# Kernel tuning notes

Hardware: AMD Instinct MI355X
Metric: run time of the kernel (lower is better)

The kernel has to match this reference:

```python
import jax, jax.numpy as jnp
import numpy as np

N = 6144      # nodes
NFEAT = 512
NHID = 256
NHEADS = 4
DHEAD = NHID // NHEADS  # 64
NEMBED = 128
NEG_INF = -9e15
LRELU_ALPHA = 0.2


def setup_inputs() -> dict:
    key = jax.random.key(0)
    k = jax.random.split(key, 8)
    x = jax.random.normal(k[0], (N, NFEAT), dtype=jnp.float32)
    adj = (jax.random.uniform(k[1], (N, N)) < 0.01).astype(jnp.int32)
    # per-head GAT params, packed over heads
    W = jax.random.normal(k[2], (NHEADS, NFEAT, DHEAD), dtype=jnp.float32) * 0.05
    a_src = jax.random.normal(k[3], (NHEADS, DHEAD), dtype=jnp.float32) * 0.05
    a_dst = jax.random.normal(k[4], (NHEADS, DHEAD), dtype=jnp.float32) * 0.05
    # output linear (init.normal_ std=0.05 per reset_parameters)
    lin_w = jax.random.normal(k[5], (NEMBED, NHID), dtype=jnp.float32) * 0.05
    lin_b = jnp.zeros((NEMBED,), dtype=jnp.float32)
    return {"x": x, "adj": adj, "W": W, "a_src": a_src, "a_dst": a_dst,
            "lin_w": lin_w, "lin_b": lin_b}


def _gat_forward(x, adj, W, a_src, a_dst, lin_w, lin_b):
    # Wh: [H, N, D]
    Wh = jnp.einsum('nf,hfd->hnd', x, W)
    # attention logits e_ij = leakyrelu(a_src.Wh_i + a_dst.Wh_j): [H, N, N]
    s = jnp.einsum('hnd,hd->hn', Wh, a_src)   # source term per node
    t = jnp.einsum('hnd,hd->hn', Wh, a_dst)   # target term per node
    e = s[:, :, None] + t[:, None, :]
    e = jax.nn.leaky_relu(e, negative_slope=LRELU_ALPHA)
    # mask by adjacency, softmax over neighbors
    e = jnp.where(adj[None, :, :] > 0, e, NEG_INF)
    attn = jax.nn.softmax(e, axis=-1)
    # aggregate and per-head ELU (concat=True GAT layer)
    h = jnp.einsum('hnm,hmd->hnd', attn, Wh)
    h = jax.nn.elu(h)
    # concat heads -> [N, NHID]
    h = jnp.transpose(h, (1, 0, 2)).reshape(N, NHID)
    # dropout is identity in eval mode; linear + ELU
    out = jax.nn.elu(h @ lin_w.T + lin_b)
    return out


def reference(x, adj, W, a_src, a_dst, lin_w, lin_b):
    return _gat_forward(x, adj, W, a_src, a_dst, lin_w, lin_b)
```

## Files before the change

kernel.cpp:

```cpp
#include <hip/hip_runtime.h>
#include <hip/hip_bf16.h>
#include <math.h>

#define N_NODES 6144
#define NFEAT 512
#define NHID 256
#define NHEADS 4
#define DHEAD 64
#define NEMBED 128
#define LRELU_ALPHA 0.2f
#define MAXC 256
#define ASTRIDE 20

__global__ __launch_bounds__(256) void gemm_scan(const float* __restrict__ x,
                                                 const float* __restrict__ W,
                                                 const float* __restrict__ a_src,
                                                 const float* __restrict__ a_dst,
                                                 const int* __restrict__ adj,
                                                 float* __restrict__ Wh,
                                                 float* __restrict__ s_arr,
                                                 float* __restrict__ t_arr,
                                                 int* __restrict__ cnt_g,
                                                 unsigned short* __restrict__ nbr_g) {
    __shared__ float As[64][ASTRIDE];
    __shared__ float Bs[16][64];
    const int tid = threadIdx.x;

    if (blockIdx.y < NHEADS) {
        const int tx = tid & 15;
        const int ty = tid >> 4;
        const int row0 = blockIdx.x * 64;
        const int h = blockIdx.y;
        const float* Bp = W + (size_t)h * NFEAT * DHEAD;

        float acc[4][4] = {};

        for (int k0 = 0; k0 < NFEAT; k0 += 16) {
            {
                const int r = tid >> 2, kq = tid & 3;
                const float4 v = *(const float4*)(x + (size_t)(row0 + r) * NFEAT + k0 + kq * 4);
                *(float4*)&As[r][kq * 4] = v;
            }
            {
                const int kk = tid >> 4, cq = tid & 15;
                const float4 v = *(const float4*)(Bp + (size_t)(k0 + kk) * DHEAD + cq * 4);
                *(float4*)&Bs[kk][cq * 4] = v;
            }
            __syncthreads();
#pragma unroll
            for (int kk = 0; kk < 16; kk++) {
                float a[4], b[4];
#pragma unroll
                for (int i = 0; i < 4; i++) a[i] = As[ty * 4 + i][kk];
#pragma unroll
                for (int j = 0; j < 4; j++) b[j] = Bs[kk][tx * 4 + j];
#pragma unroll
                for (int i = 0; i < 4; i++)
#pragma unroll
                    for (int j = 0; j < 4; j++) acc[i][j] += a[i] * b[j];
            }
            __syncthreads();
        }
#pragma unroll
        for (int i = 0; i < 4; i++) {
            const int row = row0 + ty * 4 + i;
            float4 v = make_float4(acc[i][0], acc[i][1], acc[i][2], acc[i][3]);
            *(float4*)(Wh + ((size_t)h * N_NODES + row) * DHEAD + tx * 4) = v;
        }
        float a4s[4], a4d[4];
#pragma unroll
        for (int j = 0; j < 4; j++) {
            a4s[j] = a_src[h * DHEAD + tx * 4 + j];
            a4d[j] = a_dst[h * DHEAD + tx * 4 + j];
        }
#pragma unroll
        for (int i = 0; i < 4; i++) {
            float ps = acc[i][0] * a4s[0] + acc[i][1] * a4s[1] +
                       acc[i][2] * a4s[2] + acc[i][3] * a4s[3];
            float pt = acc[i][0] * a4d[0] + acc[i][1] * a4d[1] +
                       acc[i][2] * a4d[2] + acc[i][3] * a4d[3];
#pragma unroll
            for (int off = 1; off < 16; off <<= 1) {
                ps += __shfl_xor(ps, off);
                pt += __shfl_xor(pt, off);
            }
            if (tx == 0) {
                const int row = row0 + ty * 4 + i;
                s_arr[h * N_NODES + row] = ps;
                t_arr[h * N_NODES + row] = pt;
            }
        }
    } else {
        const int r = (blockIdx.y - NHEADS) * gridDim.x + blockIdx.x;
        const int* arow = adj + (size_t)r * N_NODES;
        unsigned short* nrow = nbr_g + (size_t)r * MAXC;
        int* cp = cnt_g + r;

        int4 v[6];
#pragma unroll
        for (int it = 0; it < 6; ++it)
            v[it] = *(const int4*)(arow + it * 1024 + tid * 4);

#pragma unroll
        for (int it = 0; it < 6; ++it) {
            const int j0 = it * 1024 + tid * 4;
            const int n = (v[it].x != 0) + (v[it].y != 0) + (v[it].z != 0) + (v[it].w != 0);
            if (n) {
                int base = atomicAdd(cp, n);
                if (v[it].x) { if (base < MAXC) nrow[base] = (unsigned short)j0; ++base; }
                if (v[it].y) { if (base < MAXC) nrow[base] = (unsigned short)(j0 + 1); ++base; }
                if (v[it].z) { if (base < MAXC) nrow[base] = (unsigned short)(j0 + 2); ++base; }
                if (v[it].w) { if (base < MAXC) nrow[base] = (unsigned short)(j0 + 3); }
            }
        }
    }
}

__global__ __launch_bounds__(256) void attn_agg(const int* __restrict__ adj,
                                                const float* __restrict__ Wh,
                                                const float* __restrict__ s_arr,
                                                const float* __restrict__ t_arr,
                                                const int* __restrict__ cnt_g,
                                                const unsigned short* __restrict__ nbr_g,
                                                float* __restrict__ hcat) {
    __shared__ unsigned short nbr[MAXC];
    __shared__ float p_s[NHEADS][MAXC];
    const int i = blockIdx.x;
    const int tid = threadIdx.x;
    const int h = tid >> 6;
    const int lane = tid & 63;
    const int c = cnt_g[i];
    const float* whp = Wh + (size_t)h * N_NODES * DHEAD;

    float acc, l;
    if (c > 0 && c <= MAXC) {
        for (int k = tid; k < c; k += 256) nbr[k] = nbr_g[(size_t)i * MAXC + k];
        __syncthreads();

        const float s_h = s_arr[h * N_NODES + i];
        const float* tp = t_arr + (size_t)h * N_NODES;
        float m = -INFINITY;
        for (int k = lane; k < c; k += 64) {
            float e = s_h + tp[nbr[k]];
            e = e >= 0.0f ? e : LRELU_ALPHA * e;
            p_s[h][k] = e;
            m = fmaxf(m, e);
        }
#pragma unroll
        for (int off = 32; off > 0; off >>= 1) m = fmaxf(m, __shfl_xor(m, off));
        float ls = 0.0f;
        for (int k = lane; k < c; k += 64) {
            const float p = __expf(p_s[h][k] - m);
            p_s[h][k] = p;
            ls += p;
        }
#pragma unroll
        for (int off = 32; off > 0; off >>= 1) ls += __shfl_xor(ls, off);
        l = ls;

        float a0 = 0.f, a1 = 0.f, a2 = 0.f, a3 = 0.f;
        float a4 = 0.f, a5 = 0.f, a6 = 0.f, a7 = 0.f;
        int k = 0;
        for (; k + 8 <= c; k += 8) {
            const int j0 = nbr[k],     j1 = nbr[k + 1], j2 = nbr[k + 2], j3 = nbr[k + 3];
            const int j4 = nbr[k + 4], j5 = nbr[k + 5], j6 = nbr[k + 6], j7 = nbr[k + 7];
            const float p0 = p_s[h][k],     p1 = p_s[h][k + 1];
            const float p2 = p_s[h][k + 2], p3 = p_s[h][k + 3];
            const float p4 = p_s[h][k + 4], p5 = p_s[h][k + 5];
            const float p6 = p_s[h][k + 6], p7 = p_s[h][k + 7];
            a0 += p0 * whp[(size_t)j0 * DHEAD + lane];
            a1 += p1 * whp[(size_t)j1 * DHEAD + lane];
            a2 += p2 * whp[(size_t)j2 * DHEAD + lane];
            a3 += p3 * whp[(size_t)j3 * DHEAD + lane];
            a4 += p4 * whp[(size_t)j4 * DHEAD + lane];
            a5 += p5 * whp[(size_t)j5 * DHEAD + lane];
            a6 += p6 * whp[(size_t)j6 * DHEAD + lane];
            a7 += p7 * whp[(size_t)j7 * DHEAD + lane];
        }
        for (; k < c; k++) a0 += p_s[h][k] * whp[(size_t)nbr[k] * DHEAD + lane];
        acc = ((a0 + a1) + (a2 + a3)) + ((a4 + a5) + (a6 + a7));
    } else if (c == 0) {
        acc = 0.0f;
        for (int j = 0; j < N_NODES; j++) acc += whp[(size_t)j * DHEAD + lane];
        l = (float)N_NODES;
    } else {
        const int* arow = adj + (size_t)i * N_NODES;
        const float s_h = s_arr[h * N_NODES + i];
        const float* tp = t_arr + (size_t)h * N_NODES;
        float m = -INFINITY, ll = 0.0f;
        acc = 0.0f;
        for (int j = 0; j < N_NODES; j++) {
            if (arow[j]) {
                float e = s_h + tp[j];
                e = e >= 0.0f ? e : LRELU_ALPHA * e;
                const float m_new = fmaxf(m, e);
                const float scale = __expf(m - m_new);
                const float p = __expf(e - m_new);
                ll = ll * scale + p;
                acc = acc * scale + p * whp[(size_t)j * DHEAD + lane];
                m = m_new;
            }
        }
        l = ll;
    }
    float hv = acc / l;
    hv = hv > 0.0f ? hv : expm1f(hv);
    hcat[(size_t)i * NHID + h * DHEAD + lane] = hv;
}

__global__ __launch_bounds__(256) void out_gemm(const float* __restrict__ hcat,
                                                const float* __restrict__ lin_w,
                                                const float* __restrict__ lin_b,
                                                float* __restrict__ out) {
    __shared__ float As[64][ASTRIDE * 4];
    __shared__ float Bs[16][64];
    const int tid = threadIdx.x;
    const int tx = tid & 15;
    const int ty = tid >> 4;
    const int row0 = blockIdx.x * 64;
    const int c0 = blockIdx.y * 64;

    float acc[4][4] = {};

    for (int k0 = 0; k0 < NHID; k0 += 16) {
        {
            const int r = tid >> 2, kq = tid & 3;
            const float4 v = *(const float4*)(hcat + (size_t)(row0 + r) * NHID + k0 + kq * 4);
            *(float4*)&As[r][kq * 4] = v;
        }
        {
            const int cc = tid & 63, kq = tid >> 6;
            const float4 v = *(const float4*)(lin_w + (size_t)(c0 + cc) * NHID + k0 + kq * 4);
            Bs[kq * 4 + 0][cc] = v.x;
            Bs[kq * 4 + 1][cc] = v.y;
            Bs[kq * 4 + 2][cc] = v.z;
            Bs[kq * 4 + 3][cc] = v.w;
        }
        __syncthreads();
#pragma unroll
        for (int kk = 0; kk < 16; kk++) {
            float a[4], b[4];
#pragma unroll
            for (int i = 0; i < 4; i++) a[i] = As[ty * 4 + i][kk];
#pragma unroll
            for (int j = 0; j < 4; j++) b[j] = Bs[kk][tx * 4 + j];
#pragma unroll
            for (int i = 0; i < 4; i++)
#pragma unroll
                for (int j = 0; j < 4; j++) acc[i][j] += a[i] * b[j];
        }
        __syncthreads();
    }
#pragma unroll
    for (int i = 0; i < 4; i++) {
        const int row = row0 + ty * 4 + i;
        float v[4];
#pragma unroll
        for (int j = 0; j < 4; j++) {
            const int col = c0 + tx * 4 + j;
            float val = acc[i][j] + lin_b[col];
            v[j] = val > 0.0f ? val : expm1f(val);
        }
        *(float4*)(out + (size_t)row * NEMBED + c0 + tx * 4) =
            make_float4(v[0], v[1], v[2], v[3]);
    }
}

extern "C" void kernel_launch(void* const* d_in, const int* in_sizes, int n_in,
                              void* d_out, int out_size, void* d_ws, size_t ws_size,
                              hipStream_t stream) {
    const float* x     = (const float*)d_in[0];
    const int*   adj   = (const int*)d_in[1];
    const float* W     = (const float*)d_in[2];
    const float* a_src = (const float*)d_in[3];
    const float* a_dst = (const float*)d_in[4];
    const float* lin_w = (const float*)d_in[5];
    const float* lin_b = (const float*)d_in[6];
    float* out = (float*)d_out;

    float* Wh   = (float*)d_ws;
    float* s    = Wh + (size_t)NHEADS * N_NODES * DHEAD;
    float* t    = s + (size_t)NHEADS * N_NODES;
    float* hcat = t + (size_t)NHEADS * N_NODES;
    int* cnt_g  = (int*)(hcat + (size_t)N_NODES * NHID);
    unsigned short* nbr_g = (unsigned short*)(cnt_g + N_NODES);

    hipMemsetAsync(cnt_g, 0, N_NODES * sizeof(int), stream);
    gemm_scan<<<dim3(96, NHEADS + 64), 256, 0, stream>>>(
        x, W, a_src, a_dst, adj, Wh, s, t, cnt_g, nbr_g);
    attn_agg<<<N_NODES, 256, 0, stream>>>(adj, Wh, s, t, cnt_g, nbr_g, hcat);
    out_gemm<<<dim3(N_NODES / 64, NEMBED / 64), 256, 0, stream>>>(hcat, lin_w, lin_b, out);
}
```

Measured before the change: 287.5 us.

## Transpose GEMM A tile for vector LDS reads and batch adjacency scan rows

The x tile is stored transposed in shared memory so each thread reads four A values with a single float4 LDS load instead of four scalar loads. The grid is flattened to 1D with the 384 GEMM blocks first. Each scan block now processes three adjacency rows and prefetches the next row's int4 data while compacting the current row, cutting scan blocks from 6144 to 2048. This aims to lower LDS instruction count in the GEMM and hide global-load latency in the memory-bound adjacency scan. The cost is more registers per scan thread and bank conflicts on the scalar transposed stores.

```diff
diff --git a/kernel.cpp b/kernel.cpp
--- a/kernel.cpp
+++ b/kernel.cpp
@@ -11,6 +11,9 @@
 #define LRELU_ALPHA 0.2f
 #define MAXC 256
 #define ASTRIDE 20
+#define GEMM_BLOCKS 384
+#define SCAN_BLOCKS 2048
+#define ROWS_PER_SCAN 3
 
 __global__ __launch_bounds__(256) void gemm_scan(const float* __restrict__ x,
                                                  const float* __restrict__ W,
@@ -22,15 +25,16 @@
                                                  float* __restrict__ t_arr,
                                                  int* __restrict__ cnt_g,
                                                  unsigned short* __restrict__ nbr_g) {
-    __shared__ float As[64][ASTRIDE];
+    __shared__ float AsT[16][68];
     __shared__ float Bs[16][64];
     const int tid = threadIdx.x;
 
-    if (blockIdx.y < NHEADS) {
+    if (blockIdx.x < GEMM_BLOCKS) {
+        const int bx = blockIdx.x;
+        const int h = bx / 96;
+        const int row0 = (bx - h * 96) * 64;
         const int tx = tid & 15;
         const int ty = tid >> 4;
-        const int row0 = blockIdx.x * 64;
-        const int h = blockIdx.y;
         const float* Bp = W + (size_t)h * NFEAT * DHEAD;
 
         float acc[4][4] = {};
@@ -39,7 +43,10 @@
             {
                 const int r = tid >> 2, kq = tid & 3;
                 const float4 v = *(const float4*)(x + (size_t)(row0 + r) * NFEAT + k0 + kq * 4);
-                *(float4*)&As[r][kq * 4] = v;
+                AsT[kq * 4 + 0][r] = v.x;
+                AsT[kq * 4 + 1][r] = v.y;
+                AsT[kq * 4 + 2][r] = v.z;
+                AsT[kq * 4 + 3][r] = v.w;
             }
             {
                 const int kk = tid >> 4, cq = tid & 15;
@@ -49,11 +56,10 @@
             __syncthreads();
 #pragma unroll
             for (int kk = 0; kk < 16; kk++) {
-                float a[4], b[4];
-#pragma unroll
-                for (int i = 0; i < 4; i++) a[i] = As[ty * 4 + i][kk];
-#pragma unroll
-                for (int j = 0; j < 4; j++) b[j] = Bs[kk][tx * 4 + j];
+                const float4 av = *(const float4*)&AsT[kk][ty * 4];
+                const float4 bv = *(const float4*)&Bs[kk][tx * 4];
+                const float a[4] = {av.x, av.y, av.z, av.w};
+                const float b[4] = {bv.x, bv.y, bv.z, bv.w};
 #pragma unroll
                 for (int i = 0; i < 4; i++)
 #pragma unroll
@@ -91,27 +97,42 @@
             }
         }
     } else {
-        const int r = (blockIdx.y - NHEADS) * gridDim.x + blockIdx.x;
-        const int* arow = adj + (size_t)r * N_NODES;
-        unsigned short* nrow = nbr_g + (size_t)r * MAXC;
-        int* cp = cnt_g + r;
-
-        int4 v[6];
-#pragma unroll
-        for (int it = 0; it < 6; ++it)
-            v[it] = *(const int4*)(arow + it * 1024 + tid * 4);
-
-#pragma unroll
-        for (int it = 0; it < 6; ++it) {
-            const int j0 = it * 1024 + tid * 4;
-            const int n = (v[it].x != 0) + (v[it].y != 0) + (v[it].z != 0) + (v[it].w != 0);
-            if (n) {
-                int base = atomicAdd(cp, n);
-                if (v[it].x) { if (base < MAXC) nrow[base] = (unsigned short)j0; ++base; }
-                if (v[it].y) { if (base < MAXC) nrow[base] = (unsigned short)(j0 + 1); ++base; }
-                if (v[it].z) { if (base < MAXC) nrow[base] = (unsigned short)(j0 + 2); ++base; }
-                if (v[it].w) { if (base < MAXC) nrow[base] = (unsigned short)(j0 + 3); }
-            }
+        const int sb = blockIdx.x - GEMM_BLOCKS;
+        int r = sb * ROWS_PER_SCAN;
+        const int tid4 = tid * 4;
+
+        int4 v[6], vn[6];
+        {
+            const int* arow = adj + (size_t)r * N_NODES;
+#pragma unroll
+            for (int it = 0; it < 6; ++it)
+                v[it] = *(const int4*)(arow + it * 1024 + tid4);
+        }
+#pragma unroll
+        for (int q = 0; q < ROWS_PER_SCAN; ++q) {
+            if (q < ROWS_PER_SCAN - 1) {
+                const int* anext = adj + (size_t)(r + 1) * N_NODES;
+#pragma unroll
+                for (int it = 0; it < 6; ++it)
+                    vn[it] = *(const int4*)(anext + it * 1024 + tid4);
+            }
+            int* cp = cnt_g + r;
+            unsigned short* nrow = nbr_g + (size_t)r * MAXC;
+#pragma unroll
+            for (int it = 0; it < 6; ++it) {
+                const int j0 = it * 1024 + tid4;
+                const int n = (v[it].x != 0) + (v[it].y != 0) + (v[it].z != 0) + (v[it].w != 0);
+                if (n) {
+                    int base = atomicAdd(cp, n);
+                    if (v[it].x) { if (base < MAXC) nrow[base] = (unsigned short)j0; ++base; }
+                    if (v[it].y) { if (base < MAXC) nrow[base] = (unsigned short)(j0 + 1); ++base; }
+                    if (v[it].z) { if (base < MAXC) nrow[base] = (unsigned short)(j0 + 2); ++base; }
+                    if (v[it].w) { if (base < MAXC) nrow[base] = (unsigned short)(j0 + 3); }
+                }
+            }
+#pragma unroll
+            for (int it = 0; it < 6; ++it) v[it] = vn[it];
+            ++r;
         }
     }
 }
@@ -286,7 +307,7 @@
     unsigned short* nbr_g = (unsigned short*)(cnt_g + N_NODES);
 
     hipMemsetAsync(cnt_g, 0, N_NODES * sizeof(int), stream);
-    gemm_scan<<<dim3(96, NHEADS + 64), 256, 0, stream>>>(
+    gemm_scan<<<dim3(GEMM_BLOCKS + SCAN_BLOCKS), 256, 0, stream>>>(
         x, W, a_src, a_dst, adj, Wh, s, t, cnt_g, nbr_g);
     attn_agg<<<N_NODES, 256, 0, stream>>>(adj, Wh, s, t, cnt_g, nbr_g, hcat);
     out_gemm<<<dim3(N_NODES / 64, NEMBED / 64), 256, 0, stream>>>(hcat, lin_w, lin_b, out);
```

New measurement: 297.7 us. +3.5%, slower.
